# Optimization experiments

Measured on AMD Instinct MI355X. Metric: run time of the kernel, lower is better.

Reference implementation:

```python
import jax, jax.numpy as jnp
import numpy as np

N = 50000
E = 800000
D_IN = 64
D_OUT = 64
H = 8
R = 8  # num_relations; relation id R is reserved for self-loops
NEG_SLOPE = 0.2
EPS = 1e-10


def setup_inputs() -> dict:
    key = jax.random.key(0)
    ks = jax.random.split(key, 7)
    x = jax.random.normal(ks[0], (N, D_IN), jnp.float32)
    # xavier_uniform-like scale for W_tau, kaiming-like for query
    w_scale = (6.0 / (D_IN + D_OUT)) ** 0.5
    W_tau = jax.random.normal(ks[1], (R + 1, D_OUT, D_IN), jnp.float32) * w_scale
    query = jax.random.normal(ks[2], (R + 1, H, 2 * D_OUT // H), jnp.float32) * 0.1
    node_in = jax.random.randint(ks[3], (E,), 0, N, jnp.int32)
    node_out = jax.random.randint(ks[4], (E,), 0, N, jnp.int32)
    relation = jax.random.randint(ks[5], (E,), 0, R, jnp.int32)
    edge_weight = jax.random.uniform(ks[6], (E,), jnp.float32)
    return {"x": x, "W_tau": W_tau, "query": query, "node_in": node_in,
            "node_out": node_out, "relation": relation, "edge_weight": edge_weight}


def reference(x, W_tau, query, node_in, node_out, relation, edge_weight):
    n_node = x.shape[0]
    rp1, d_out, _ = W_tau.shape  # num_relations + 1
    n_head = query.shape[1]

    # append self-loop edges with relation id = num_relations, weight 1
    self_idx = jnp.arange(n_node, dtype=node_in.dtype)
    ni = jnp.concatenate([node_in, self_idx])            # [M]
    no = jnp.concatenate([node_out, self_idx])           # [M]
    rel = jnp.concatenate([relation, jnp.full((n_node,), rp1 - 1, dtype=relation.dtype)])
    ew = jnp.concatenate([edge_weight, jnp.ones((n_node,), edge_weight.dtype)])[:, None]  # [M,1]

    # per-relation linear transform of all nodes: [R+1, N, D_out]
    hidden = jnp.einsum('rdi,ni->rnd', W_tau, x)

    # gather endpoint features per edge (relation-specific)
    h_in = hidden[rel, ni]    # [M, D_out]
    h_out = hidden[rel, no]   # [M, D_out]
    m = h_in.shape[0]

    # interleaved stack then head split, matching torch stack(dim=-1).view
    key_feat = jnp.stack([h_in, h_out], axis=-1).reshape(m, n_head, -1)  # [M,H,2*D/H]
    w = jnp.einsum('mhd,mhd->mh', query[rel], key_feat)                  # [M,H]
    w = jax.nn.leaky_relu(w, NEG_SLOPE)

    # segment softmax (stabilized by per-node max), normalizer is scatter-MEAN (faithful)
    mx = jax.ops.segment_max(w, no, num_segments=n_node)[no]
    att = jnp.exp(w - mx) * ew                                           # [M,H]
    cnt = jax.ops.segment_sum(jnp.ones((m,), x.dtype), no, num_segments=n_node)  # [N]
    norm = (jax.ops.segment_sum(att, no, num_segments=n_node) / cnt[:, None])[no]
    att = att / (norm + EPS)

    value = h_in.reshape(m, n_head, d_out // n_head)                     # [M,H,D/H]
    msg = (att[..., None] * value).reshape(m, d_out)                     # [M,D_out]

    # aggregate: scatter-mean over destination nodes, then ReLU (combine)
    update = jax.ops.segment_sum(msg, no, num_segments=n_node) / cnt[:, None]
    return jax.nn.relu(update)
```

## Files before the change

kernel.cpp:

```cpp
#include <hip/hip_runtime.h>
#include <math.h>

#define N_NODES 50000
#define N_EDGES 800000
#define DOUT 64
#define NHEAD 8
#define RP1 9
#define NEG_SLOPE 0.2f
#define EPS_F 1e-10f
#define M_TOT (N_EDGES + N_NODES)
#define NW (RP1 * DOUT * DOUT)

#define SUBSH 6
#define NSUB ((N_NODES + 63) >> SUBSH)
#define SEGCAP 1536
#define EPB 4096
#define CHUNKS ((M_TOT + EPB - 1) / EPB)
#define K1B ((N_NODES + 127) / 128)

typedef __attribute__((ext_vector_type(8))) short bf16x8;
typedef __attribute__((ext_vector_type(4))) float f32x4;

__device__ __forceinline__ unsigned short f2bf(float f) {
    unsigned int u = __float_as_uint(f);
    unsigned int r = (u + 0x7FFFu + ((u >> 16) & 1u)) >> 16;
    return (unsigned short)r;
}
__device__ __forceinline__ float bf2f(unsigned short s) {
    return __uint_as_float(((unsigned int)s) << 16);
}

__global__ __launch_bounds__(256) void kprep2(const float* __restrict__ W,
                                              unsigned short* __restrict__ Wb,
                                              int* __restrict__ subcursor) {
    int m = blockIdx.x * 256 + threadIdx.x;
    if (m < NW / 4) {
        int i = m * 4;
        float4 v = *(const float4*)(W + i);
        ushort4 o; o.x = f2bf(v.x); o.y = f2bf(v.y); o.z = f2bf(v.z); o.w = f2bf(v.w);
        *(ushort4*)(Wb + i) = o;
    }
    if (m < NSUB) subcursor[m] = 0;
}

__global__ __launch_bounds__(512) void kbig(const float* __restrict__ x,
                                            const unsigned short* __restrict__ Wb,
                                            unsigned short* __restrict__ hiddenb,
                                            const int* __restrict__ node_in,
                                            const int* __restrict__ node_out,
                                            const int* __restrict__ relation,
                                            const float* __restrict__ edge_w,
                                            int* __restrict__ subcursor,
                                            int2* __restrict__ seg) {
    __shared__ union SM {
        unsigned short st[8 * 16 * 72];
        struct { int cnt[NSUB]; int base[NSUB]; } f;
    } sm;
    const int t = threadIdx.x;

    if (blockIdx.x >= K1B) {
        const int chunk = blockIdx.x - K1B;
        const int m0 = chunk * EPB;
        for (int s2 = t; s2 < NSUB; s2 += 512) sm.f.cnt[s2] = 0;
        __syncthreads();
#pragma unroll
        for (int it = 0; it < EPB / 512; it++) {
            int m = m0 + it * 512 + t;
            if (m < M_TOT) {
                int no = (m < N_EDGES) ? node_out[m] : (m - N_EDGES);
                atomicAdd(&sm.f.cnt[no >> SUBSH], 1);
            }
        }
        __syncthreads();
        for (int s2 = t; s2 < NSUB; s2 += 512) {
            int c = sm.f.cnt[s2];
            sm.f.base[s2] = (c > 0) ? atomicAdd(&subcursor[s2], c) : 0;
        }
        __syncthreads();
        for (int s2 = t; s2 < NSUB; s2 += 512) sm.f.cnt[s2] = 0;
        __syncthreads();
#pragma unroll
        for (int it = 0; it < EPB / 512; it++) {
            int m = m0 + it * 512 + t;
            if (m < M_TOT) {
                int no, ni, rl; float ew;
                if (m < N_EDGES) {
                    no = node_out[m]; ni = node_in[m];
                    rl = relation[m]; ew = edge_w[m];
                } else {
                    no = m - N_EDGES; ni = no; rl = RP1 - 1; ew = 1.0f;
                }
                int s2 = no >> SUBSH;
                int r = atomicAdd(&sm.f.cnt[s2], 1);
                int pos = sm.f.base[s2] + r;
                if (pos < SEGCAP) {
                    int2 v;
                    v.x = ni | (rl << 16) | ((no & 63) << 20);
                    v.y = __float_as_int(ew);
                    seg[(size_t)s2 * SEGCAP + pos] = v;
                }
            }
        }
        return;
    }

    const int bx = blockIdx.x;
    const int wv = t >> 6, lane = t & 63;
    const int quad = lane >> 4, l16 = lane & 15;
    const int base = bx * 128 + wv * 16;

    int arow = base + l16;
    if (arow >= N_NODES) arow = N_NODES - 1;
    const float* xr = x + (size_t)arow * 64 + quad * 8;
    const float4 f0 = *(const float4*)(xr + 0);
    const float4 f1 = *(const float4*)(xr + 4);
    const float4 f2 = *(const float4*)(xr + 32);
    const float4 f3 = *(const float4*)(xr + 36);
    bf16x8 a0, a1;
    a0[0] = (short)f2bf(f0.x); a0[1] = (short)f2bf(f0.y);
    a0[2] = (short)f2bf(f0.z); a0[3] = (short)f2bf(f0.w);
    a0[4] = (short)f2bf(f1.x); a0[5] = (short)f2bf(f1.y);
    a0[6] = (short)f2bf(f1.z); a0[7] = (short)f2bf(f1.w);
    a1[0] = (short)f2bf(f2.x); a1[1] = (short)f2bf(f2.y);
    a1[2] = (short)f2bf(f2.z); a1[3] = (short)f2bf(f2.w);
    a1[4] = (short)f2bf(f3.x); a1[5] = (short)f2bf(f3.y);
    a1[6] = (short)f2bf(f3.z); a1[7] = (short)f2bf(f3.w);

    unsigned short* sw = &sm.st[wv * 16 * 72];

    for (int r = 0; r < RP1; r++) {
        const unsigned short* Wr = Wb + r * 4096;
        f32x4 acc[4];
#pragma unroll
        for (int dt = 0; dt < 4; dt++) {
            const bf16x8 b0 = *(const bf16x8*)(Wr + (dt * 16 + l16) * 64 + quad * 8);
            const bf16x8 b1 = *(const bf16x8*)(Wr + (dt * 16 + l16) * 64 + quad * 8 + 32);
            f32x4 c = {0.f, 0.f, 0.f, 0.f};
            c = __builtin_amdgcn_mfma_f32_16x16x32_bf16(a0, b0, c, 0, 0, 0);
            c = __builtin_amdgcn_mfma_f32_16x16x32_bf16(a1, b1, c, 0, 0, 0);
            acc[dt] = c;
        }
#pragma unroll
        for (int dt = 0; dt < 4; dt++) {
#pragma unroll
            for (int v = 0; v < 4; v++) {
                sw[(quad * 4 + v) * 72 + dt * 16 + l16] = f2bf(acc[dt][v]);
            }
        }
        __threadfence_block();
#pragma unroll
        for (int q = 0; q < 2; q++) {
            int cid = q * 64 + lane;
            int row = cid >> 3;
            int ch = cid & 7;
            int n = base + row;
            if (n < N_NODES) {
                bf16x8 v = *(const bf16x8*)(sw + row * 72 + ch * 8);
                *(bf16x8*)(hiddenb + ((size_t)r * N_NODES + n) * 64 + ch * 8) = v;
            }
        }
        __threadfence_block();
    }
}

__global__ __launch_bounds__(512) void k3_seg(const unsigned short* __restrict__ hiddenb,
                                              const float* __restrict__ query,
                                              const int2* __restrict__ seg,
                                              const int* __restrict__ subcursor,
                                              float* __restrict__ out) {
    __shared__ float qe[RP1 * 64];
    __shared__ float qo[RP1 * 64];
    __shared__ int2  smeta[SEGCAP];
    __shared__ int cnt[64], start[64], cnt2[64];
    __shared__ float bho[8][2][72];

    const int t = threadIdx.x;
    const int s = blockIdx.x;
    const int scnt = min(subcursor[s], SEGCAP);

    const int i0 = t, i1 = t + 512, i2 = t + 1024;
    int2 ev0, ev1, ev2;
    if (i0 < scnt) ev0 = seg[(size_t)s * SEGCAP + i0];
    if (i1 < scnt) ev1 = seg[(size_t)s * SEGCAP + i1];
    if (i2 < scnt) ev2 = seg[(size_t)s * SEGCAP + i2];

    for (int q = t; q < RP1 * 64; q += 512) {
        int j = q & 7, rh = q >> 3;
        qe[q] = query[rh * 16 + 2 * j];
        qo[q] = query[rh * 16 + 2 * j + 1];
    }
    if (t < 64) { cnt[t] = 0; cnt2[t] = 0; }
    __syncthreads();

    if (i0 < scnt) atomicAdd(&cnt[(ev0.x >> 20) & 63], 1);
    if (i1 < scnt) atomicAdd(&cnt[(ev1.x >> 20) & 63], 1);
    if (i2 < scnt) atomicAdd(&cnt[(ev2.x >> 20) & 63], 1);
    __syncthreads();

    if (t < 64) {
        int v = cnt[t];
        int sc = v;
#pragma unroll
        for (int d = 1; d < 64; d <<= 1) {
            int o = __shfl_up(sc, d);
            if (t >= d) sc += o;
        }
        start[t] = sc - v;
    }
    __syncthreads();

    if (i0 < scnt) {
        int nol = (ev0.x >> 20) & 63;
        smeta[start[nol] + atomicAdd(&cnt2[nol], 1)] = ev0;
    }
    if (i1 < scnt) {
        int nol = (ev1.x >> 20) & 63;
        smeta[start[nol] + atomicAdd(&cnt2[nol], 1)] = ev1;
    }
    if (i2 < scnt) {
        int nol = (ev2.x >> 20) & 63;
        smeta[start[nol] + atomicAdd(&cnt2[nol], 1)] = ev2;
    }
    __syncthreads();

    const int wv = t >> 6, lane = t & 63;
    const int e_lo = lane >> 3, h = lane & 7;
    const int prel = lane >> 3, ph = lane & 7;

    for (int k = 0; k < 4; k++) {
        const int nAl = (k * 8 + wv) * 2, nBl = nAl + 1;
        const int nA = (s << SUBSH) + nAl, nB = nA + 1;
        if (nA >= N_NODES) continue;

        {
            const bf16x8 ra = *(const bf16x8*)(hiddenb + ((size_t)(prel * N_NODES + nA)) * 64 + ph * 8);
            const bf16x8 rb = *(const bf16x8*)(hiddenb + ((size_t)(prel * N_NODES + nB)) * 64 + ph * 8);
            bf16x8 r8 = ra;
            if (lane < 16) {
                int n8 = (lane < 8) ? nA : nB;
                r8 = *(const bf16x8*)(hiddenb + ((size_t)(8 * N_NODES + n8)) * 64 + (lane & 7) * 8);
            }
            const float* qop = &qo[(prel * 8 + ph) * 8];
            float da = 0.f, db = 0.f;
#pragma unroll
            for (int j = 0; j < 8; j++) {
                da += qop[j] * bf2f((unsigned short)ra[j]);
                db += qop[j] * bf2f((unsigned short)rb[j]);
            }
            bho[wv][0][prel * 8 + ph] = da;
            bho[wv][1][prel * 8 + ph] = db;
            if (lane < 16) {
                const float* q8p = &qo[(64 + (lane & 7)) * 8];
                float d8 = 0.f;
#pragma unroll
                for (int j = 0; j < 8; j++) d8 += q8p[j] * bf2f((unsigned short)r8[j]);
                bho[wv][(lane < 8) ? 0 : 1][64 + (lane & 7)] = d8;
            }
        }
        __threadfence_block();

        const int cA = cnt[nAl], cB = cnt[nBl];
        const int stA = start[nAl], stB = start[nBl];
        const float degA = (float)cA, degB = (float)cB;
        const int cM = (cA > cB) ? cA : cB;

        float accA[8] = {0.f, 0.f, 0.f, 0.f, 0.f, 0.f, 0.f, 0.f};
        float accB[8] = {0.f, 0.f, 0.f, 0.f, 0.f, 0.f, 0.f, 0.f};
        float spA = 0.f, spB = 0.f;

        for (int j0 = 0; j0 < cM; j0 += 32) {
            bf16x8 rA[4], rB[4];
            int relA[4], relB[4]; float ewA[4], ewB[4];
#pragma unroll
            for (int p = 0; p < 4; p++) {
                const int sa = j0 + p * 8 + e_lo;
                if (sa < cA) {
                    int2 mv = smeta[stA + sa];
                    int ni = mv.x & 0xffff;
                    int rl = min((mv.x >> 16) & 15, RP1 - 1);
                    relA[p] = rl; ewA[p] = __int_as_float(mv.y);
                    rA[p] = *(const bf16x8*)(hiddenb + ((size_t)(rl * N_NODES + ni)) * 64 + h * 8);
                }
                if (sa < cB) {
                    int2 mv = smeta[stB + sa];
                    int ni = mv.x & 0xffff;
                    int rl = min((mv.x >> 16) & 15, RP1 - 1);
                    relB[p] = rl; ewB[p] = __int_as_float(mv.y);
                    rB[p] = *(const bf16x8*)(hiddenb + ((size_t)(rl * N_NODES + ni)) * 64 + h * 8);
                }
            }
#pragma unroll
            for (int p = 0; p < 4; p++) {
                const int sa = j0 + p * 8 + e_lo;
                if (sa < cA) {
                    const float* qp = &qe[(relA[p] * 8 + h) * 8];
                    float hif[8];
#pragma unroll
                    for (int j = 0; j < 8; j++) hif[j] = bf2f((unsigned short)rA[p][j]);
                    float wp = bho[wv][0][relA[p] * 8 + h];
#pragma unroll
                    for (int j = 0; j < 8; j++) wp += qp[j] * hif[j];
                    wp = (wp > 0.f) ? wp : NEG_SLOPE * wp;
                    float pa = __expf(wp) * ewA[p];
#pragma unroll
                    for (int j = 0; j < 8; j++) accA[j] += pa * hif[j];
                    spA += pa;
                }
                if (sa < cB) {
                    const float* qp = &qe[(relB[p] * 8 + h) * 8];
                    float hif[8];
#pragma unroll
                    for (int j = 0; j < 8; j++) hif[j] = bf2f((unsigned short)rB[p][j]);
                    float wp = bho[wv][1][relB[p] * 8 + h];
#pragma unroll
                    for (int j = 0; j < 8; j++) wp += qp[j] * hif[j];
                    wp = (wp > 0.f) ? wp : NEG_SLOPE * wp;
                    float pa = __expf(wp) * ewB[p];
#pragma unroll
                    for (int j = 0; j < 8; j++) accB[j] += pa * hif[j];
                    spB += pa;
                }
            }
        }

#pragma unroll
        for (int j = 0; j < 8; j++) {
            accA[j] += __shfl_xor(accA[j], 8);
            accA[j] += __shfl_xor(accA[j], 16);
            accA[j] += __shfl_xor(accA[j], 32);
            accB[j] += __shfl_xor(accB[j], 8);
            accB[j] += __shfl_xor(accB[j], 16);
            accB[j] += __shfl_xor(accB[j], 32);
        }
        spA += __shfl_xor(spA, 8); spA += __shfl_xor(spA, 16); spA += __shfl_xor(spA, 32);
        spB += __shfl_xor(spB, 8); spB += __shfl_xor(spB, 16); spB += __shfl_xor(spB, 32);

        if (lane < 8) {
            const float sc = 1.f / ((spA / degA + EPS_F) * degA);
            float4 o0, o1;
            o0.x = fmaxf(accA[0] * sc, 0.f); o0.y = fmaxf(accA[1] * sc, 0.f);
            o0.z = fmaxf(accA[2] * sc, 0.f); o0.w = fmaxf(accA[3] * sc, 0.f);
            o1.x = fmaxf(accA[4] * sc, 0.f); o1.y = fmaxf(accA[5] * sc, 0.f);
            o1.z = fmaxf(accA[6] * sc, 0.f); o1.w = fmaxf(accA[7] * sc, 0.f);
            float* op = out + (size_t)nA * 64 + lane * 8;
            *(float4*)(op) = o0; *(float4*)(op + 4) = o1;
        } else if (lane < 16) {
            const float sc = 1.f / ((spB / degB + EPS_F) * degB);
            float4 o0, o1;
            o0.x = fmaxf(accB[0] * sc, 0.f); o0.y = fmaxf(accB[1] * sc, 0.f);
            o0.z = fmaxf(accB[2] * sc, 0.f); o0.w = fmaxf(accB[3] * sc, 0.f);
            o1.x = fmaxf(accB[4] * sc, 0.f); o1.y = fmaxf(accB[5] * sc, 0.f);
            o1.z = fmaxf(accB[6] * sc, 0.f); o1.w = fmaxf(accB[7] * sc, 0.f);
            float* op = out + (size_t)nB * 64 + (lane - 8) * 8;
            *(float4*)(op) = o0; *(float4*)(op + 4) = o1;
        }
    }
}

extern "C" void kernel_launch(void* const* d_in, const int* in_sizes, int n_in,
                              void* d_out, int out_size, void* d_ws, size_t ws_size,
                              hipStream_t stream) {
    const float* x        = (const float*)d_in[0];
    const float* W_tau    = (const float*)d_in[1];
    const float* query    = (const float*)d_in[2];
    const int*   node_in  = (const int*)d_in[3];
    const int*   node_out = (const int*)d_in[4];
    const int*   relation = (const int*)d_in[5];
    const float* edge_w   = (const float*)d_in[6];
    float* out = (float*)d_out;

    char* ws = (char*)d_ws;
    unsigned short* hiddenb   = (unsigned short*)(ws);
    unsigned short* Wb        = (unsigned short*)(ws + 57600000);
    int2*           seg       = (int2*)(ws + 57673728);
    int*            subcursor = (int*)(ws + 67282944);

    kprep2<<<(NW / 4 + 255) / 256, 256, 0, stream>>>(W_tau, Wb, subcursor);

    kbig<<<K1B + CHUNKS, 512, 0, stream>>>(x, Wb, hiddenb, node_in, node_out,
                                           relation, edge_w, subcursor, seg);

    k3_seg<<<NSUB, 512, 0, stream>>>(hiddenb, query, seg, subcursor, out);
}
```

Before: 165.6 us.

## Precompute per-node destination query dot products in GEMM kernel epilogue

Moves the per-destination-node query·h_out dot products (all relations and heads) out of the segment kernel and into the hidden-projection kernel's epilogue, where the freshly computed bf16 tile already sits in shared memory. The results are written to a new fp32 [N,72] workspace buffer, and the segment kernel loads them with one float4 read per lane instead of gathering hidden rows for 9 relations and recomputing. This drops redundant gathers and math from the attention kernel. In exchange it adds global writes and reads of about 14 MB plus extra epilogue work and shared memory in the GEMM kernel.

Measured after the change: 160.7 us. 1.03x faster.

```diff
diff --git a/kernel.cpp b/kernel.cpp
--- a/kernel.cpp
+++ b/kernel.cpp
@@ -51,11 +51,14 @@
                                             const int* __restrict__ relation,
                                             const float* __restrict__ edge_w,
                                             int* __restrict__ subcursor,
-                                            int2* __restrict__ seg) {
+                                            int2* __restrict__ seg,
+                                            const float* __restrict__ query,
+                                            float* __restrict__ hout) {
     __shared__ union SM {
         unsigned short st[8 * 16 * 72];
         struct { int cnt[NSUB]; int base[NSUB]; } f;
     } sm;
+    __shared__ float qoq[RP1 * 64];
     const int t = threadIdx.x;
 
     if (blockIdx.x >= K1B) {
@@ -103,6 +106,11 @@
         }
         return;
     }
+
+    for (int q = t; q < RP1 * 64; q += 512) {
+        qoq[q] = query[(q >> 3) * 16 + 2 * (q & 7) + 1];
+    }
+    __syncthreads();
 
     const int bx = blockIdx.x;
     const int wv = t >> 6, lane = t & 63;
@@ -159,6 +167,22 @@
                 *(bf16x8*)(hiddenb + ((size_t)r * N_NODES + n) * 64 + ch * 8) = v;
             }
         }
+        {
+            const int nl = lane >> 2;
+            const int h0 = (lane & 3) * 2;
+            const unsigned short* hrow = sw + nl * 72;
+            const float* q0 = &qoq[(r * 8 + h0) * 8];
+            float d0 = 0.f, d1 = 0.f;
+#pragma unroll
+            for (int j = 0; j < 8; j++) {
+                d0 += q0[j]     * bf2f(hrow[h0 * 8 + j]);
+                d1 += q0[8 + j] * bf2f(hrow[h0 * 8 + 8 + j]);
+            }
+            int n = base + nl;
+            if (n < N_NODES) {
+                *(float2*)(hout + (size_t)n * 72 + r * 8 + h0) = make_float2(d0, d1);
+            }
+        }
         __threadfence_block();
     }
 }
@@ -167,12 +191,12 @@
                                               const float* __restrict__ query,
                                               const int2* __restrict__ seg,
                                               const int* __restrict__ subcursor,
+                                              const float* __restrict__ hout,
                                               float* __restrict__ out) {
     __shared__ float qe[RP1 * 64];
-    __shared__ float qo[RP1 * 64];
     __shared__ int2  smeta[SEGCAP];
     __shared__ int cnt[64], start[64], cnt2[64];
-    __shared__ float bho[8][2][72];
+    __shared__ __align__(16) float bho[8][144];
 
     const int t = threadIdx.x;
     const int s = blockIdx.x;
@@ -187,7 +211,6 @@
     for (int q = t; q < RP1 * 64; q += 512) {
         int j = q & 7, rh = q >> 3;
         qe[q] = query[rh * 16 + 2 * j];
-        qo[q] = query[rh * 16 + 2 * j + 1];
     }
     if (t < 64) { cnt[t] = 0; cnt2[t] = 0; }
     __syncthreads();
@@ -225,37 +248,15 @@
 
     const int wv = t >> 6, lane = t & 63;
     const int e_lo = lane >> 3, h = lane & 7;
-    const int prel = lane >> 3, ph = lane & 7;
 
     for (int k = 0; k < 4; k++) {
         const int nAl = (k * 8 + wv) * 2, nBl = nAl + 1;
         const int nA = (s << SUBSH) + nAl, nB = nA + 1;
         if (nA >= N_NODES) continue;
 
-        {
-            const bf16x8 ra = *(const bf16x8*)(hiddenb + ((size_t)(prel * N_NODES + nA)) * 64 + ph * 8);
-            const bf16x8 rb = *(const bf16x8*)(hiddenb + ((size_t)(prel * N_NODES + nB)) * 64 + ph * 8);
-            bf16x8 r8 = ra;
-            if (lane < 16) {
-                int n8 = (lane < 8) ? nA : nB;
-                r8 = *(const bf16x8*)(hiddenb + ((size_t)(8 * N_NODES + n8)) * 64 + (lane & 7) * 8);
-            }
-            const float* qop = &qo[(prel * 8 + ph) * 8];
-            float da = 0.f, db = 0.f;
-#pragma unroll
-            for (int j = 0; j < 8; j++) {
-                da += qop[j] * bf2f((unsigned short)ra[j]);
-                db += qop[j] * bf2f((unsigned short)rb[j]);
-            }
-            bho[wv][0][prel * 8 + ph] = da;
-            bho[wv][1][prel * 8 + ph] = db;
-            if (lane < 16) {
-                const float* q8p = &qo[(64 + (lane & 7)) * 8];
-                float d8 = 0.f;
-#pragma unroll
-                for (int j = 0; j < 8; j++) d8 += q8p[j] * bf2f((unsigned short)r8[j]);
-                bho[wv][(lane < 8) ? 0 : 1][64 + (lane & 7)] = d8;
-            }
+        if (lane < 36) {
+            float4 v = *(const float4*)(hout + (size_t)nA * 72 + lane * 4);
+            *(float4*)(&bho[wv][lane * 4]) = v;
         }
         __threadfence_block();
 
@@ -297,7 +298,7 @@
                     float hif[8];
 #pragma unroll
                     for (int j = 0; j < 8; j++) hif[j] = bf2f((unsigned short)rA[p][j]);
-                    float wp = bho[wv][0][relA[p] * 8 + h];
+                    float wp = bho[wv][relA[p] * 8 + h];
 #pragma unroll
                     for (int j = 0; j < 8; j++) wp += qp[j] * hif[j];
                     wp = (wp > 0.f) ? wp : NEG_SLOPE * wp;
@@ -311,7 +312,7 @@
                     float hif[8];
 #pragma unroll
                     for (int j = 0; j < 8; j++) hif[j] = bf2f((unsigned short)rB[p][j]);
-                    float wp = bho[wv][1][relB[p] * 8 + h];
+                    float wp = bho[wv][72 + relB[p] * 8 + h];
 #pragma unroll
                     for (int j = 0; j < 8; j++) wp += qp[j] * hif[j];
                     wp = (wp > 0.f) ? wp : NEG_SLOPE * wp;
@@ -374,11 +375,13 @@
     unsigned short* Wb        = (unsigned short*)(ws + 57600000);
     int2*           seg       = (int2*)(ws + 57673728);
     int*            subcursor = (int*)(ws + 67282944);
+    float*          hout      = (float*)(ws + 67286080);
 
     kprep2<<<(NW / 4 + 255) / 256, 256, 0, stream>>>(W_tau, Wb, subcursor);
 
     kbig<<<K1B + CHUNKS, 512, 0, stream>>>(x, Wb, hiddenb, node_in, node_out,
-                                           relation, edge_w, subcursor, seg);
-
-    k3_seg<<<NSUB, 512, 0, stream>>>(hiddenb, query, seg, subcursor, out);
-}
+                                           relation, edge_w, subcursor, seg,
+                                           query, hout);
+
+    k3_seg<<<NSUB, 512, 0, stream>>>(hiddenb, query, seg, subcursor, hout, out);
+}
```
